# Optimization experiments

Hardware: AMD Instinct MI355X
Metric: run time of the kernel (lower is better)

## Reference

```python
import jax, jax.numpy as jnp
import numpy as np

NH, HS, K = 32, 2048, 16
HD = HS // NH
B, L = 4, 2048
EPS = 1e-6

def _ln(x, gamma, beta):
    mu = x.mean(-1, keepdims=True)
    var = x.var(-1, keepdims=True)  # ddof=0 == torch unbiased=False
    return gamma * ((x - mu) / jnp.sqrt(var + EPS)) + beta

def _ln_fused_l2_bwd(x, target, gamma, beta):
    D = x.shape[-1]
    mu = x.mean(-1, keepdims=True)
    std = jnp.sqrt(x.var(-1, keepdims=True) + EPS)
    xh = (x - mu) / std
    gxh = (gamma * xh + beta - target) * gamma
    return (D * gxh - gxh.sum(-1, keepdims=True) - xh * (gxh * xh).sum(-1, keepdims=True)) / (D * std)

def setup_inputs() -> dict:
    key = jax.random.key(0)
    ks = jax.random.split(key, 8)
    s = 0.02
    return {
        'hidden_states': jax.random.normal(ks[0], (B, L, HS), jnp.float32),
        'position_ids': jnp.tile(jnp.arange(L, dtype=jnp.int32)[None], (B, 1)),
        'q_w': jax.random.normal(ks[1], (HS, HS), jnp.float32) * s,
        'k_w': jax.random.normal(ks[2], (HS, HS), jnp.float32) * s,
        'v_w': jax.random.normal(ks[3], (HS, HS), jnp.float32) * s,
        'o_w': jax.random.normal(ks[4], (HS, HS), jnp.float32) * s,
        'W1': jax.random.normal(ks[5], (NH, HD, HD), jnp.float32) * s,
        'b1': jnp.zeros((NH, 1, HD), jnp.float32),
        'ttt_norm_weight': jnp.ones((NH, HD), jnp.float32),
        'ttt_norm_bias': jnp.zeros((NH, HD), jnp.float32),
        'ttt_lr_weight': jax.random.normal(ks[6], (NH, 1, HS), jnp.float32) * s,
        'ttt_lr_bias': jnp.zeros((NH, 1), jnp.float32),
        'learnable_token_idx': jnp.zeros((K,), jnp.float32),
        'post_norm_weight': jnp.ones((HS,), jnp.float32),
        'post_norm_bias': jnp.zeros((HS,), jnp.float32),
    }

def _forward(hidden_states, q_w, k_w, v_w, o_w, W1, b1, ttt_norm_weight,
             ttt_norm_bias, ttt_lr_weight, ttt_lr_bias, learnable_token_idx,
             post_norm_weight, post_norm_bias):
    Bb, Ll, _ = hidden_states.shape
    NM = Ll // K

    def proj_heads(w):
        return (hidden_states @ w.T).reshape(Bb, Ll, NH, HD).transpose(0, 2, 1, 3)

    XQ = proj_heads(q_w).reshape(Bb, NH, NM, K, HD)
    XK = proj_heads(k_w).reshape(Bb, NH, NM, K, HD)
    XV = proj_heads(v_w).reshape(Bb, NH, NM, K, HD)
    X = hidden_states.reshape(Bb, NM, K, HS)

    # eta: learned per-token lr gate, [B,nh,NM,K,K]
    ttt_lr = jnp.einsum('bnkc,hdc->bhnkd', X, ttt_lr_weight) + ttt_lr_bias.reshape(1, NH, 1, 1, 1)
    ttt_lr_eta = jax.nn.sigmoid(ttt_lr).transpose(0, 1, 2, 4, 3) / HD  # ttt_base_lr = 1.0
    token_idx = jnp.clip(1.0 / jnp.arange(1, K + 1, dtype=jnp.float32) + learnable_token_idx, 0.0, None)
    eta = token_idx.reshape(1, 1, 1, K, 1) * ttt_lr_eta

    ln_w = ttt_norm_weight.reshape(NH, 1, HD)
    ln_b = ttt_norm_bias.reshape(NH, 1, HD)

    def step(carry, x):
        W1_s, b1_s = carry                 # [B,nh,hd,hd], [B,nh,1,hd]
        xq, xk, xv, eta_mb = x             # [B,nh,K,hd], eta_mb [B,nh,K,K]
        Z1 = xk @ W1_s + b1_s
        grad = _ln_fused_l2_bwd(Z1, xv - xk, ln_w, ln_b)
        Attn1 = jnp.tril(xq @ xk.swapaxes(-1, -2))
        b1_bar = b1_s - jnp.tril(eta_mb) @ grad
        Z1_bar = xq @ W1_s - (eta_mb * Attn1) @ grad + b1_bar
        last_eta = eta_mb[:, :, -1, :, None]  # [B,nh,K,1]
        W1_new = W1_s - (last_eta * xk).swapaxes(-1, -2) @ grad
        b1_new = b1_s - jnp.sum(last_eta * grad, axis=-2, keepdims=True)
        out = xq + _ln(Z1_bar, ln_w, ln_b)
        return (W1_new, b1_new), out

    init = (jnp.tile(W1[None], (Bb, 1, 1, 1)), jnp.tile(b1[None], (Bb, 1, 1, 1)))
    xs = (XQ.transpose(2, 0, 1, 3, 4), XK.transpose(2, 0, 1, 3, 4),
          XV.transpose(2, 0, 1, 3, 4), eta.transpose(2, 0, 1, 3, 4))
    _, ys = jax.lax.scan(step, init, xs)          # [NM,B,nh,K,hd]
    out = ys.transpose(1, 0, 3, 2, 4).reshape(Bb, Ll, HS)
    out = _ln(out, post_norm_weight, post_norm_bias)  # post_norm (eps 1e-6)
    return out @ o_w.T

def reference(hidden_states, position_ids, q_w, k_w, v_w, o_w, W1, b1,
              ttt_norm_weight, ttt_norm_bias, ttt_lr_weight, ttt_lr_bias,
              learnable_token_idx, post_norm_weight, post_norm_bias):
    del position_ids  # unused in the shown forward (rope never applied)
    return _forward(hidden_states, q_w, k_w, v_w, o_w, W1, b1, ttt_norm_weight,
                    ttt_norm_bias, ttt_lr_weight, ttt_lr_bias, learnable_token_idx,
                    post_norm_weight, post_norm_bias)
```

## Files before the change

kernel.cpp:

```cpp
#include <hip/hip_runtime.h>

typedef unsigned short u16;
typedef unsigned int u32;
typedef __bf16 bf16_t;
typedef bf16_t bf16x4 __attribute__((ext_vector_type(4)));
typedef bf16_t bf16x8 __attribute__((ext_vector_type(8)));
typedef float f32x4 __attribute__((ext_vector_type(4)));
typedef u16 u16x4 __attribute__((ext_vector_type(4)));
typedef u16 u16x8 __attribute__((ext_vector_type(8)));
typedef short s16x4 __attribute__((ext_vector_type(4)));

#define B_   4
#define L_   2048
#define HS_  2048
#define NH_  32
#define HD_  64
#define KK_  16
#define NM_  128
#define M_   (B_*L_)

__device__ __forceinline__ u16 f2bf(float f) {
  unsigned u = __float_as_uint(f);
  u += 0x7FFFu + ((u >> 16) & 1u);
  return (u16)(u >> 16);
}
__device__ __forceinline__ float bf2f(u16 u) {
  return __uint_as_float(((unsigned)u) << 16);
}
__device__ __forceinline__ u16 f2bfh(float f) {
  __bf16 h = (__bf16)f;
  return __builtin_bit_cast(u16, h);
}
__device__ __forceinline__ s16x4 pk4(float a, float b, float c, float d) {
  bf16x4 v;
  v[0] = (__bf16)a; v[1] = (__bf16)b; v[2] = (__bf16)c; v[3] = (__bf16)d;
  return __builtin_bit_cast(s16x4, v);
}

__device__ __forceinline__ f32x4 mfma16(s16x4 a, s16x4 b, f32x4 c) {
  return __builtin_amdgcn_mfma_f32_16x16x16bf16_1k(a, b, c, 0, 0, 0);
}

template <int CTRL>
__device__ __forceinline__ float dpp_add(float v) {
  int t = __builtin_amdgcn_update_dpp(0, __builtin_bit_cast(int, v), CTRL, 0xF, 0xF, true);
  return v + __builtin_bit_cast(float, t);
}
template <int CTRL>
__device__ __forceinline__ f32x4 dpp_add4(f32x4 v) {
  f32x4 r;
#pragma unroll
  for (int i = 0; i < 4; ++i) r[i] = dpp_add<CTRL>(v[i]);
  return r;
}
__device__ __forceinline__ f32x4 row_reduce16(f32x4 v) {
  v = dpp_add4<0x121>(v);
  v = dpp_add4<0x122>(v);
  v = dpp_add4<0x124>(v);
  v = dpp_add4<0x128>(v);
  return v;
}

__global__ __launch_bounds__(256) void cast_f32_bf16(const float* __restrict__ in,
                                                     u16* __restrict__ out, int n) {
  int i = (blockIdx.x * 256 + threadIdx.x) * 8;
  if (i >= n) return;
  float4 a = *(const float4*)(in + i);
  float4 b = *(const float4*)(in + i + 4);
  u16x8 o;
  o[0]=f2bf(a.x); o[1]=f2bf(a.y); o[2]=f2bf(a.z); o[3]=f2bf(a.w);
  o[4]=f2bf(b.x); o[5]=f2bf(b.y); o[6]=f2bf(b.z); o[7]=f2bf(b.w);
  *(u16x8*)(out + i) = o;
}

#define BM 128
#define BN 128
#define BK 32
#define LDT 40

template <bool BF16OUT>
__global__ __launch_bounds__(256) void gemm_nt(const u16* __restrict__ A,
                                               const u16* __restrict__ Bt,
                                               void* __restrict__ Cv,
                                               int M, int N, int K) {
  __shared__ u16 As[BM * LDT];
  __shared__ u16 Bs[BN * LDT];
  int tid  = threadIdx.x;
  int lane = tid & 63, wave = tid >> 6;
  int quad = lane >> 4, l16 = lane & 15;
  int bM = blockIdx.x * BM, bN = blockIdx.y * BN;
  int wM = (wave >> 1) * 64, wN = (wave & 1) * 64;
  int r0 = tid >> 2, c0 = (tid & 3) * 8;
  const u16* Ap = A + (size_t)bM * K;
  const u16* Bp = Bt + (size_t)bN * K;
  f32x4 acc[4][4] = {};
  u16x8 pa0 = *(const u16x8*)(Ap + (size_t)r0 * K + c0);
  u16x8 pa1 = *(const u16x8*)(Ap + (size_t)(r0 + 64) * K + c0);
  u16x8 pb0 = *(const u16x8*)(Bp + (size_t)r0 * K + c0);
  u16x8 pb1 = *(const u16x8*)(Bp + (size_t)(r0 + 64) * K + c0);
  int nk = K / BK;
  for (int kt = 0; kt < nk; ++kt) {
    *(u16x8*)&As[r0 * LDT + c0]        = pa0;
    *(u16x8*)&As[(r0 + 64) * LDT + c0] = pa1;
    *(u16x8*)&Bs[r0 * LDT + c0]        = pb0;
    *(u16x8*)&Bs[(r0 + 64) * LDT + c0] = pb1;
    __syncthreads();
    if (kt + 1 < nk) {
      int k0 = (kt + 1) * BK + c0;
      pa0 = *(const u16x8*)(Ap + (size_t)r0 * K + k0);
      pa1 = *(const u16x8*)(Ap + (size_t)(r0 + 64) * K + k0);
      pb0 = *(const u16x8*)(Bp + (size_t)r0 * K + k0);
      pb1 = *(const u16x8*)(Bp + (size_t)(r0 + 64) * K + k0);
    }
    bf16x8 af[4], bfr[4];
#pragma unroll
    for (int i = 0; i < 4; ++i) {
      u16x8 t = *(const u16x8*)&As[(wM + i * 16 + l16) * LDT + quad * 8];
      af[i] = __builtin_bit_cast(bf16x8, t);
    }
#pragma unroll
    for (int j = 0; j < 4; ++j) {
      u16x8 t = *(const u16x8*)&Bs[(wN + j * 16 + l16) * LDT + quad * 8];
      bfr[j] = __builtin_bit_cast(bf16x8, t);
    }
#pragma unroll
    for (int i = 0; i < 4; ++i) {
#pragma unroll
      for (int j = 0; j < 4; ++j)
        acc[i][j] = __builtin_amdgcn_mfma_f32_16x16x32_bf16(af[i], bfr[j], acc[i][j], 0, 0, 0);
    }
    __syncthreads();
  }
#pragma unroll
  for (int i = 0; i < 4; ++i) {
#pragma unroll
    for (int j = 0; j < 4; ++j) {
      int row = bM + wM + i * 16 + quad * 4;
      int col = bN + wN + j * 16 + l16;
      if (BF16OUT) {
        u16* cp = (u16*)Cv + (size_t)row * N + col;
#pragma unroll
        for (int r = 0; r < 4; ++r) cp[(size_t)r * N] = f2bf(acc[i][j][r]);
      } else {
        float* cp = (float*)Cv + (size_t)row * N + col;
#pragma unroll
        for (int r = 0; r < 4; ++r) cp[(size_t)r * N] = acc[i][j][r];
      }
    }
  }
}

__global__ __launch_bounds__(256) void sig_kernel(const u16* __restrict__ hsb,
                                                  const u16* __restrict__ lrwb,
                                                  const float* __restrict__ lrb,
                                                  float* __restrict__ Sig) {
  __shared__ u16 Bs[32 * LDT];
  int tid = threadIdx.x;
  int lane = tid & 63, wave = tid >> 6;
  int quad = lane >> 4, l16 = lane & 15;
  int m0 = blockIdx.x * 64 + wave * 16;
  f32x4 acc0 = {}, acc1 = {};
  for (int kt = 0; kt < HS_ / BK; ++kt) {
    int k0 = kt * BK;
    if (tid < 128) {
      int r = tid >> 2, c8 = (tid & 3) * 8;
      *(u16x8*)&Bs[r * LDT + c8] = *(const u16x8*)(lrwb + (size_t)r * HS_ + k0 + c8);
    }
    __syncthreads();
    u16x8 ta = *(const u16x8*)(hsb + (size_t)(m0 + l16) * HS_ + k0 + quad * 8);
    u16x8 t0 = *(const u16x8*)&Bs[l16 * LDT + quad * 8];
    u16x8 t1 = *(const u16x8*)&Bs[(16 + l16) * LDT + quad * 8];
    bf16x8 af  = __builtin_bit_cast(bf16x8, ta);
    bf16x8 bf0 = __builtin_bit_cast(bf16x8, t0);
    bf16x8 bf1 = __builtin_bit_cast(bf16x8, t1);
    acc0 = __builtin_amdgcn_mfma_f32_16x16x32_bf16(af, bf0, acc0, 0, 0, 0);
    acc1 = __builtin_amdgcn_mfma_f32_16x16x32_bf16(af, bf1, acc1, 0, 0, 0);
    __syncthreads();
  }
#pragma unroll
  for (int j = 0; j < 2; ++j) {
    f32x4 a = j ? acc1 : acc0;
    int h = j * 16 + l16;
    float bias = lrb[h];
#pragma unroll
    for (int r = 0; r < 4; ++r) {
      int m = m0 + quad * 4 + r;
      float v = a[r] + bias;
      float s = (1.f / (1.f + expf(-v))) * (1.f / 64.f);
      Sig[(size_t)m * NH_ + h] = s;
    }
  }
}

__global__ __launch_bounds__(64, 1) void ttt_scan_wave(
    const u16* __restrict__ XQ, const u16* __restrict__ XK, const u16* __restrict__ XV,
    const float* __restrict__ Sig, const float* __restrict__ W1_0, const float* __restrict__ b1_0,
    const float* __restrict__ lnw, const float* __restrict__ lnb, const float* __restrict__ lti,
    float* __restrict__ Y) {
  __shared__ __align__(16) u16 xkT[64 * 20];
  __shared__ __align__(16) float diffS[16 * 68];

  int lane = threadIdx.x;
  int quad = lane >> 4, l16 = lane & 15;
  int bh = blockIdx.x, b = bh >> 5, h = bh & 31;

  f32x4 m2[4][4];
  {
    const float* wsrc = W1_0 + (size_t)h * 4096;
#pragma unroll
    for (int c = 0; c < 4; ++c)
#pragma unroll
      for (int a = 0; a < 4; ++a)
#pragma unroll
        for (int r = 0; r < 4; ++r)
          m2[c][a][r] = wsrc[(size_t)(c * 16 + quad * 4 + r) * 64 + a * 16 + l16];
  }

  f32x4 b1r, gam, bet;
#pragma unroll
  for (int a = 0; a < 4; ++a) {
    b1r[a] = b1_0[h * 64 + a * 16 + l16];
    gam[a] = lnw[h * 64 + a * 16 + l16];
    bet[a] = lnb[h * 64 + a * 16 + l16];
  }
  float tokL  = fmaxf(1.0f / (float)(l16 + 1) + lti[l16], 0.0f);
  float tok15 = fmaxf(1.0f / 16.0f + lti[15], 0.0f);

  size_t gb = ((size_t)(b * L_ + l16)) * HS_ + h * HD_ + quad * 4;
  const float* sigp = Sig + (size_t)(b * L_ + quad * 4) * NH_ + h;

  u16x4 cxk[4], cxq[4], cxv[4];
  f32x4 csig;
#pragma unroll
  for (int c = 0; c < 4; ++c) {
    cxk[c] = *(const u16x4*)(XK + gb + c * 16);
    cxq[c] = *(const u16x4*)(XQ + gb + c * 16);
    cxv[c] = *(const u16x4*)(XV + gb + c * 16);
  }
#pragma unroll
  for (int r = 0; r < 4; ++r) csig[r] = sigp[(size_t)r * NH_];

  for (int n = 0; n < NM_; ++n) {
    s16x4 fwB[4][4];
#pragma unroll
    for (int c = 0; c < 4; ++c)
#pragma unroll
      for (int a = 0; a < 4; ++a)
        fwB[c][a] = pk4(m2[c][a][0], m2[c][a][1], m2[c][a][2], m2[c][a][3]);

#pragma unroll
    for (int c = 0; c < 4; ++c) {
      f32x4 dv;
#pragma unroll
      for (int j = 0; j < 4; ++j) dv[j] = bf2f(cxv[c][j]) - bf2f(cxk[c][j]);
      *(f32x4*)&diffS[l16 * 68 + c * 16 + quad * 4] = dv;
#pragma unroll
      for (int j = 0; j < 4; ++j)
        xkT[(c * 16 + quad * 4 + j) * 20 + l16] = f2bfh(-tok15 * bf2f(cxk[c][j]));
    }

    s16x4 fxk[4], fxq[4];
#pragma unroll
    for (int c = 0; c < 4; ++c) {
      fxk[c] = __builtin_bit_cast(s16x4, cxk[c]);
      fxq[c] = __builtin_bit_cast(s16x4, cxq[c]);
    }
    f32x4 sigc = csig;

    if (n + 1 < NM_) {
      size_t g = gb + (size_t)(n + 1) * KK_ * HS_;
#pragma unroll
      for (int c = 0; c < 4; ++c) {
        cxk[c] = *(const u16x4*)(XK + g + c * 16);
        cxq[c] = *(const u16x4*)(XQ + g + c * 16);
        cxv[c] = *(const u16x4*)(XV + g + c * 16);
      }
#pragma unroll
      for (int r = 0; r < 4; ++r)
        csig[r] = sigp[(size_t)((n + 1) * KK_ + r) * NH_];
    }

    f32x4 z1[4] = {}, zq4[4] = {}, atT = {};
#pragma unroll
    for (int c = 0; c < 4; ++c) {
      atT = mfma16(fxk[c], fxq[c], atT);
#pragma unroll
      for (int a = 0; a < 4; ++a) {
        z1[a]  = mfma16(fxk[c], fwB[c][a], z1[a]);
        zq4[a] = mfma16(fxq[c], fwB[c][a], zq4[a]);
      }
    }

    float cf[4];
#pragma unroll
    for (int r = 0; r < 4; ++r)
      cf[r] = (quad * 4 + r <= l16) ? -tokL * (1.0f + atT[r]) : 0.0f;
    s16x4 fA = pk4(cf[0], cf[1], cf[2], cf[3]);

#pragma unroll
    for (int a = 0; a < 4; ++a)
#pragma unroll
      for (int r = 0; r < 4; ++r) z1[a][r] += b1r[a];
    f32x4 s1 = z1[0] + z1[1] + z1[2] + z1[3];
    f32x4 s2 = z1[0] * z1[0] + z1[1] * z1[1] + z1[2] * z1[2] + z1[3] * z1[3];
    s1 = row_reduce16(s1);
    s2 = row_reduce16(s2);
    f32x4 mu, rstd;
#pragma unroll
    for (int r = 0; r < 4; ++r) {
      mu[r] = s1[r] * (1.0f / 64.0f);
      float var = s2[r] * (1.0f / 64.0f) - mu[r] * mu[r];
      rstd[r] = 1.0f / sqrtf(var + 1e-6f);
    }

    f32x4 dd[4];
#pragma unroll
    for (int a = 0; a < 4; ++a)
#pragma unroll
      for (int r = 0; r < 4; ++r)
        dd[a][r] = diffS[(quad * 4 + r) * 68 + a * 16 + l16];

    f32x4 xh[4], gxh[4], t1v = {}, t2v = {};
#pragma unroll
    for (int a = 0; a < 4; ++a) {
#pragma unroll
      for (int r = 0; r < 4; ++r) {
        xh[a][r]  = (z1[a][r] - mu[r]) * rstd[r];
        gxh[a][r] = (gam[a] * xh[a][r] + bet[a] - dd[a][r]) * gam[a];
      }
      t1v = t1v + gxh[a];
      t2v = t2v + gxh[a] * xh[a];
    }
    t1v = row_reduce16(t1v);
    t2v = row_reduce16(t2v);

    s16x4 fG[4];
    float bs[4];
#pragma unroll
    for (int a = 0; a < 4; ++a) {
      float sg[4];
#pragma unroll
      for (int r = 0; r < 4; ++r) {
        float g = (64.0f * gxh[a][r] - t1v[r] - xh[a][r] * t2v[r]) * (rstd[r] * (1.0f / 64.0f));
        sg[r] = sigc[r] * g;
      }
      fG[a] = pk4(sg[0], sg[1], sg[2], sg[3]);
      bs[a] = sg[0] + sg[1] + sg[2] + sg[3];
    }
#pragma unroll
    for (int a = 0; a < 4; ++a) {
      bs[a] += __shfl_xor(bs[a], 16, 64);
      bs[a] += __shfl_xor(bs[a], 32, 64);
    }

    f32x4 zb[4];
#pragma unroll
    for (int a = 0; a < 4; ++a) {
      zb[a] = mfma16(fA, fG[a], zq4[a]);
#pragma unroll
      for (int r = 0; r < 4; ++r) zb[a][r] += b1r[a];
    }
#pragma unroll
    for (int a = 0; a < 4; ++a) b1r[a] -= tok15 * bs[a];

    {
      s16x4 fX[4];
#pragma unroll
      for (int c = 0; c < 4; ++c)
        fX[c] = *(const s16x4*)&xkT[(c * 16 + l16) * 20 + quad * 4];
#pragma unroll
      for (int c = 0; c < 4; ++c)
#pragma unroll
        for (int a = 0; a < 4; ++a)
          m2[c][a] = mfma16(fX[c], fG[a], m2[c][a]);
    }

    f32x4 w1s = zb[0] + zb[1] + zb[2] + zb[3];
    f32x4 w2s = zb[0] * zb[0] + zb[1] * zb[1] + zb[2] * zb[2] + zb[3] * zb[3];
    w1s = row_reduce16(w1s);
    w2s = row_reduce16(w2s);
#pragma unroll
    for (int r = 0; r < 4; ++r) {
      float mu2 = w1s[r] * (1.0f / 64.0f);
      float var2 = w2s[r] * (1.0f / 64.0f) - mu2 * mu2;
      float rstd2 = 1.0f / sqrtf(var2 + 1e-6f);
      float* yp = Y + ((size_t)(b * L_ + n * KK_ + quad * 4 + r)) * HS_ + h * HD_ + l16;
#pragma unroll
      for (int a = 0; a < 4; ++a)
        yp[a * 16] = gam[a] * ((zb[a][r] - mu2) * rstd2) + bet[a];
    }
  }
}

__global__ __launch_bounds__(256) void postnorm(const float* __restrict__ Yin,
                                                const u16* __restrict__ XQr,
                                                const float* __restrict__ w,
                                                const float* __restrict__ bb,
                                                u16* __restrict__ Yn) {
  __shared__ float red[8];
  int row = blockIdx.x, tid = threadIdx.x;
  const float* x = Yin + (size_t)row * HS_ + tid * 8;
  float4 v0 = *(const float4*)(x);
  float4 v1 = *(const float4*)(x + 4);
  u16x8 xqv = *(const u16x8*)(XQr + (size_t)row * HS_ + tid * 8);
  float vals[8] = {v0.x, v0.y, v0.z, v0.w, v1.x, v1.y, v1.z, v1.w};
#pragma unroll
  for (int t = 0; t < 8; ++t) vals[t] += bf2f(xqv[t]);
  float s = 0.f, ss = 0.f;
#pragma unroll
  for (int t = 0; t < 8; ++t) { s += vals[t]; ss += vals[t] * vals[t]; }
#pragma unroll
  for (int m = 32; m > 0; m >>= 1) { s += __shfl_xor(s, m, 64); ss += __shfl_xor(ss, m, 64); }
  int wave = tid >> 6, lane = tid & 63;
  if (lane == 0) { red[wave] = s; red[4 + wave] = ss; }
  __syncthreads();
  float S  = red[0] + red[1] + red[2] + red[3];
  float SS = red[4] + red[5] + red[6] + red[7];
  float mu = S * (1.f / 2048.f);
  float var = SS * (1.f / 2048.f) - mu * mu;
  float rstd = 1.f / sqrtf(var + 1e-6f);
  const float* wp = w + tid * 8;
  const float* bp = bb + tid * 8;
  u16x8 o;
#pragma unroll
  for (int t = 0; t < 8; ++t) o[t] = f2bf(wp[t] * ((vals[t] - mu) * rstd) + bp[t]);
  *(u16x8*)(Yn + (size_t)row * HS_ + tid * 8) = o;
}

extern "C" void kernel_launch(void* const* d_in, const int* in_sizes, int n_in,
                              void* d_out, int out_size, void* d_ws, size_t ws_size,
                              hipStream_t stream) {
  (void)in_sizes; (void)n_in; (void)out_size; (void)ws_size;
  const float* hidden = (const float*)d_in[0];
  const float* q_w = (const float*)d_in[2];
  const float* k_w = (const float*)d_in[3];
  const float* v_w = (const float*)d_in[4];
  const float* o_w = (const float*)d_in[5];
  const float* W1  = (const float*)d_in[6];
  const float* b1i = (const float*)d_in[7];
  const float* lnw = (const float*)d_in[8];
  const float* lnb = (const float*)d_in[9];
  const float* lrw = (const float*)d_in[10];
  const float* lrb = (const float*)d_in[11];
  const float* lti = (const float*)d_in[12];
  const float* pnw = (const float*)d_in[13];
  const float* pnb = (const float*)d_in[14];
  float* out = (float*)d_out;

  char* w = (char*)d_ws;
  u16* hsb  = (u16*)w;  w += (size_t)16777216 * 2;
  u16* wb   = (u16*)w;  w += (size_t)4194304 * 2;
  u16* lrwb = (u16*)w;  w += (size_t)65536 * 2;
  u16* XQb  = (u16*)w;  w += (size_t)16777216 * 2;
  u16* XKb  = (u16*)w;  w += (size_t)16777216 * 2;
  u16* XVb  = (u16*)w;  w += (size_t)16777216 * 2;
  float* Sg = (float*)w; w += (size_t)M_ * NH_ * 4;
  u16* Yn = hsb;

  cast_f32_bf16<<<8192, 256, 0, stream>>>(hidden, hsb, 16777216);
  cast_f32_bf16<<<32, 256, 0, stream>>>(lrw, lrwb, 65536);

  sig_kernel<<<128, 256, 0, stream>>>(hsb, lrwb, lrb, Sg);

  dim3 gg(M_ / BM, HS_ / BN);
  cast_f32_bf16<<<2048, 256, 0, stream>>>(q_w, wb, 4194304);
  gemm_nt<true><<<gg, 256, 0, stream>>>(hsb, wb, XQb, M_, HS_, HS_);
  cast_f32_bf16<<<2048, 256, 0, stream>>>(k_w, wb, 4194304);
  gemm_nt<true><<<gg, 256, 0, stream>>>(hsb, wb, XKb, M_, HS_, HS_);
  cast_f32_bf16<<<2048, 256, 0, stream>>>(v_w, wb, 4194304);
  gemm_nt<true><<<gg, 256, 0, stream>>>(hsb, wb, XVb, M_, HS_, HS_);

  ttt_scan_wave<<<128, 64, 0, stream>>>(XQb, XKb, XVb, Sg, W1, b1i, lnw, lnb, lti, out);

  postnorm<<<8192, 256, 0, stream>>>(out, XQb, pnw, pnb, Yn);

  cast_f32_bf16<<<2048, 256, 0, stream>>>(o_w, wb, 4194304);
  gemm_nt<false><<<gg, 256, 0, stream>>>(Yn, wb, out, M_, HS_, HS_);
}
```

Measured before the change: 893.0 us.

## Interleave two independent head scans per wave to hide serial latency

Each wave now carries two (batch, head) recurrent chains and interleaves their per-chunk work, with the grid halved from 128 to 64 single-wave blocks. The aim is to fill the dependency stalls of the serial scan (MFMA chains, row reductions, shuffles, LDS round trips) with independent work from the second chain. The cost is roughly double the register footprint, since the W1 state alone takes 128 VGPRs per chain, which risks spills. It also halves the number of CUs in use, so each wave must gain enough ILP to offset running on half as many units.

Result: slower. 1.253 ms (+40.3%).

```diff
diff --git a/kernel.cpp b/kernel.cpp
--- a/kernel.cpp
+++ b/kernel.cpp
@@ -197,15 +197,23 @@
     const float* __restrict__ Sig, const float* __restrict__ W1_0, const float* __restrict__ b1_0,
     const float* __restrict__ lnw, const float* __restrict__ lnb, const float* __restrict__ lti,
     float* __restrict__ Y) {
-  __shared__ __align__(16) u16 xkT[64 * 20];
-  __shared__ __align__(16) float diffS[16 * 68];
+  __shared__ __align__(16) u16 xkT[2][64 * 20];
+  __shared__ __align__(16) float diffS[2][16 * 68];
 
   int lane = threadIdx.x;
   int quad = lane >> 4, l16 = lane & 15;
-  int bh = blockIdx.x, b = bh >> 5, h = bh & 31;
-
-  f32x4 m2[4][4];
-  {
+
+  f32x4 m2[2][4][4];
+  f32x4 b1r[2], gam[2], bet[2];
+  size_t gb[2];
+  const float* sigp[2];
+  float* yb[2];
+  u16x4 cxk[2][4], cxq[2][4], cxv[2][4];
+  f32x4 csig[2];
+
+#pragma unroll
+  for (int ch = 0; ch < 2; ++ch) {
+    int bh = blockIdx.x * 2 + ch, b = bh >> 5, h = bh & 31;
     const float* wsrc = W1_0 + (size_t)h * 4096;
 #pragma unroll
     for (int c = 0; c < 4; ++c)
@@ -213,181 +221,203 @@
       for (int a = 0; a < 4; ++a)
 #pragma unroll
         for (int r = 0; r < 4; ++r)
-          m2[c][a][r] = wsrc[(size_t)(c * 16 + quad * 4 + r) * 64 + a * 16 + l16];
+          m2[ch][c][a][r] = wsrc[(size_t)(c * 16 + quad * 4 + r) * 64 + a * 16 + l16];
+#pragma unroll
+    for (int a = 0; a < 4; ++a) {
+      b1r[ch][a] = b1_0[h * 64 + a * 16 + l16];
+      gam[ch][a] = lnw[h * 64 + a * 16 + l16];
+      bet[ch][a] = lnb[h * 64 + a * 16 + l16];
+    }
+    gb[ch]   = ((size_t)(b * L_ + l16)) * HS_ + h * HD_ + quad * 4;
+    sigp[ch] = Sig + (size_t)(b * L_ + quad * 4) * NH_ + h;
+    yb[ch]   = Y + (size_t)(b * L_) * HS_ + h * HD_ + l16;
+#pragma unroll
+    for (int c = 0; c < 4; ++c) {
+      cxk[ch][c] = *(const u16x4*)(XK + gb[ch] + c * 16);
+      cxq[ch][c] = *(const u16x4*)(XQ + gb[ch] + c * 16);
+      cxv[ch][c] = *(const u16x4*)(XV + gb[ch] + c * 16);
+    }
+#pragma unroll
+    for (int r = 0; r < 4; ++r) csig[ch][r] = sigp[ch][(size_t)r * NH_];
   }
 
-  f32x4 b1r, gam, bet;
-#pragma unroll
-  for (int a = 0; a < 4; ++a) {
-    b1r[a] = b1_0[h * 64 + a * 16 + l16];
-    gam[a] = lnw[h * 64 + a * 16 + l16];
-    bet[a] = lnb[h * 64 + a * 16 + l16];
-  }
   float tokL  = fmaxf(1.0f / (float)(l16 + 1) + lti[l16], 0.0f);
   float tok15 = fmaxf(1.0f / 16.0f + lti[15], 0.0f);
 
-  size_t gb = ((size_t)(b * L_ + l16)) * HS_ + h * HD_ + quad * 4;
-  const float* sigp = Sig + (size_t)(b * L_ + quad * 4) * NH_ + h;
-
-  u16x4 cxk[4], cxq[4], cxv[4];
-  f32x4 csig;
-#pragma unroll
-  for (int c = 0; c < 4; ++c) {
-    cxk[c] = *(const u16x4*)(XK + gb + c * 16);
-    cxq[c] = *(const u16x4*)(XQ + gb + c * 16);
-    cxv[c] = *(const u16x4*)(XV + gb + c * 16);
-  }
-#pragma unroll
-  for (int r = 0; r < 4; ++r) csig[r] = sigp[(size_t)r * NH_];
-
   for (int n = 0; n < NM_; ++n) {
-    s16x4 fwB[4][4];
-#pragma unroll
-    for (int c = 0; c < 4; ++c)
+    s16x4 fwB[2][4][4];
+#pragma unroll
+    for (int ch = 0; ch < 2; ++ch)
+#pragma unroll
+      for (int c = 0; c < 4; ++c)
+#pragma unroll
+        for (int a = 0; a < 4; ++a)
+          fwB[ch][c][a] = pk4(m2[ch][c][a][0], m2[ch][c][a][1], m2[ch][c][a][2], m2[ch][c][a][3]);
+
+#pragma unroll
+    for (int ch = 0; ch < 2; ++ch)
+#pragma unroll
+      for (int c = 0; c < 4; ++c) {
+        f32x4 dv;
+#pragma unroll
+        for (int j = 0; j < 4; ++j) dv[j] = bf2f(cxv[ch][c][j]) - bf2f(cxk[ch][c][j]);
+        *(f32x4*)&diffS[ch][l16 * 68 + c * 16 + quad * 4] = dv;
+#pragma unroll
+        for (int j = 0; j < 4; ++j)
+          xkT[ch][(c * 16 + quad * 4 + j) * 20 + l16] = f2bfh(-tok15 * bf2f(cxk[ch][c][j]));
+      }
+
+    f32x4 sigc[2] = {csig[0], csig[1]};
+
+    f32x4 z1[2][4] = {}, zq4[2][4] = {}, atT[2] = {};
+#pragma unroll
+    for (int ch = 0; ch < 2; ++ch)
+#pragma unroll
+      for (int c = 0; c < 4; ++c) {
+        s16x4 fxk = __builtin_bit_cast(s16x4, cxk[ch][c]);
+        s16x4 fxq = __builtin_bit_cast(s16x4, cxq[ch][c]);
+        atT[ch] = mfma16(fxk, fxq, atT[ch]);
+#pragma unroll
+        for (int a = 0; a < 4; ++a) {
+          z1[ch][a]  = mfma16(fxk, fwB[ch][c][a], z1[ch][a]);
+          zq4[ch][a] = mfma16(fxq, fwB[ch][c][a], zq4[ch][a]);
+        }
+      }
+
+    if (n + 1 < NM_) {
+#pragma unroll
+      for (int ch = 0; ch < 2; ++ch) {
+        size_t g = gb[ch] + (size_t)(n + 1) * KK_ * HS_;
+#pragma unroll
+        for (int c = 0; c < 4; ++c) {
+          cxk[ch][c] = *(const u16x4*)(XK + g + c * 16);
+          cxq[ch][c] = *(const u16x4*)(XQ + g + c * 16);
+          cxv[ch][c] = *(const u16x4*)(XV + g + c * 16);
+        }
+#pragma unroll
+        for (int r = 0; r < 4; ++r)
+          csig[ch][r] = sigp[ch][(size_t)((n + 1) * KK_ + r) * NH_];
+      }
+    }
+
+    s16x4 fA[2];
+#pragma unroll
+    for (int ch = 0; ch < 2; ++ch) {
+      float cf[4];
+#pragma unroll
+      for (int r = 0; r < 4; ++r)
+        cf[r] = (quad * 4 + r <= l16) ? -tokL * (1.0f + atT[ch][r]) : 0.0f;
+      fA[ch] = pk4(cf[0], cf[1], cf[2], cf[3]);
+    }
+
+    f32x4 mu[2], rstd[2];
+#pragma unroll
+    for (int ch = 0; ch < 2; ++ch) {
 #pragma unroll
       for (int a = 0; a < 4; ++a)
-        fwB[c][a] = pk4(m2[c][a][0], m2[c][a][1], m2[c][a][2], m2[c][a][3]);
-
-#pragma unroll
-    for (int c = 0; c < 4; ++c) {
-      f32x4 dv;
-#pragma unroll
-      for (int j = 0; j < 4; ++j) dv[j] = bf2f(cxv[c][j]) - bf2f(cxk[c][j]);
-      *(f32x4*)&diffS[l16 * 68 + c * 16 + quad * 4] = dv;
-#pragma unroll
-      for (int j = 0; j < 4; ++j)
-        xkT[(c * 16 + quad * 4 + j) * 20 + l16] = f2bfh(-tok15 * bf2f(cxk[c][j]));
-    }
-
-    s16x4 fxk[4], fxq[4];
-#pragma unroll
-    for (int c = 0; c < 4; ++c) {
-      fxk[c] = __builtin_bit_cast(s16x4, cxk[c]);
-      fxq[c] = __builtin_bit_cast(s16x4, cxq[c]);
-    }
-    f32x4 sigc = csig;
-
-    if (n + 1 < NM_) {
-      size_t g = gb + (size_t)(n + 1) * KK_ * HS_;
-#pragma unroll
-      for (int c = 0; c < 4; ++c) {
-        cxk[c] = *(const u16x4*)(XK + g + c * 16);
-        cxq[c] = *(const u16x4*)(XQ + g + c * 16);
-        cxv[c] = *(const u16x4*)(XV + g + c * 16);
-      }
-#pragma unroll
-      for (int r = 0; r < 4; ++r)
-        csig[r] = sigp[(size_t)((n + 1) * KK_ + r) * NH_];
-    }
-
-    f32x4 z1[4] = {}, zq4[4] = {}, atT = {};
-#pragma unroll
-    for (int c = 0; c < 4; ++c) {
-      atT = mfma16(fxk[c], fxq[c], atT);
+#pragma unroll
+        for (int r = 0; r < 4; ++r) z1[ch][a][r] += b1r[ch][a];
+      f32x4 s1 = z1[ch][0] + z1[ch][1] + z1[ch][2] + z1[ch][3];
+      f32x4 s2 = z1[ch][0] * z1[ch][0] + z1[ch][1] * z1[ch][1]
+               + z1[ch][2] * z1[ch][2] + z1[ch][3] * z1[ch][3];
+      s1 = row_reduce16(s1);
+      s2 = row_reduce16(s2);
+#pragma unroll
+      for (int r = 0; r < 4; ++r) {
+        mu[ch][r] = s1[r] * (1.0f / 64.0f);
+        float var = s2[r] * (1.0f / 64.0f) - mu[ch][r] * mu[ch][r];
+        rstd[ch][r] = 1.0f / sqrtf(var + 1e-6f);
+      }
+    }
+
+    f32x4 xh[2][4], gxh[2][4], t1v[2], t2v[2];
+#pragma unroll
+    for (int ch = 0; ch < 2; ++ch) {
+      f32x4 a1 = {}, a2 = {};
 #pragma unroll
       for (int a = 0; a < 4; ++a) {
-        z1[a]  = mfma16(fxk[c], fwB[c][a], z1[a]);
-        zq4[a] = mfma16(fxq[c], fwB[c][a], zq4[a]);
-      }
-    }
-
-    float cf[4];
-#pragma unroll
-    for (int r = 0; r < 4; ++r)
-      cf[r] = (quad * 4 + r <= l16) ? -tokL * (1.0f + atT[r]) : 0.0f;
-    s16x4 fA = pk4(cf[0], cf[1], cf[2], cf[3]);
-
-#pragma unroll
-    for (int a = 0; a < 4; ++a)
-#pragma unroll
-      for (int r = 0; r < 4; ++r) z1[a][r] += b1r[a];
-    f32x4 s1 = z1[0] + z1[1] + z1[2] + z1[3];
-    f32x4 s2 = z1[0] * z1[0] + z1[1] * z1[1] + z1[2] * z1[2] + z1[3] * z1[3];
-    s1 = row_reduce16(s1);
-    s2 = row_reduce16(s2);
-    f32x4 mu, rstd;
-#pragma unroll
-    for (int r = 0; r < 4; ++r) {
-      mu[r] = s1[r] * (1.0f / 64.0f);
-      float var = s2[r] * (1.0f / 64.0f) - mu[r] * mu[r];
-      rstd[r] = 1.0f / sqrtf(var + 1e-6f);
-    }
-
-    f32x4 dd[4];
-#pragma unroll
-    for (int a = 0; a < 4; ++a)
-#pragma unroll
-      for (int r = 0; r < 4; ++r)
-        dd[a][r] = diffS[(quad * 4 + r) * 68 + a * 16 + l16];
-
-    f32x4 xh[4], gxh[4], t1v = {}, t2v = {};
-#pragma unroll
-    for (int a = 0; a < 4; ++a) {
+        f32x4 dd;
+#pragma unroll
+        for (int r = 0; r < 4; ++r)
+          dd[r] = diffS[ch][(quad * 4 + r) * 68 + a * 16 + l16];
+#pragma unroll
+        for (int r = 0; r < 4; ++r) {
+          xh[ch][a][r]  = (z1[ch][a][r] - mu[ch][r]) * rstd[ch][r];
+          gxh[ch][a][r] = (gam[ch][a] * xh[ch][a][r] + bet[ch][a] - dd[r]) * gam[ch][a];
+        }
+        a1 = a1 + gxh[ch][a];
+        a2 = a2 + gxh[ch][a] * xh[ch][a];
+      }
+      t1v[ch] = row_reduce16(a1);
+      t2v[ch] = row_reduce16(a2);
+    }
+
+    s16x4 fG[2][4];
+    f32x4 bsv[2];
+#pragma unroll
+    for (int ch = 0; ch < 2; ++ch) {
+#pragma unroll
+      for (int a = 0; a < 4; ++a) {
+        float sg[4];
+#pragma unroll
+        for (int r = 0; r < 4; ++r) {
+          float g = (64.0f * gxh[ch][a][r] - t1v[ch][r] - xh[ch][a][r] * t2v[ch][r])
+                    * (rstd[ch][r] * (1.0f / 64.0f));
+          sg[r] = sigc[ch][r] * g;
+        }
+        fG[ch][a] = pk4(sg[0], sg[1], sg[2], sg[3]);
+        bsv[ch][a] = sg[0] + sg[1] + sg[2] + sg[3];
+      }
+#pragma unroll
+      for (int a = 0; a < 4; ++a) {
+        bsv[ch][a] += __shfl_xor(bsv[ch][a], 16, 64);
+        bsv[ch][a] += __shfl_xor(bsv[ch][a], 32, 64);
+      }
+    }
+
+    f32x4 zb[2][4];
+#pragma unroll
+    for (int ch = 0; ch < 2; ++ch) {
+#pragma unroll
+      for (int a = 0; a < 4; ++a) {
+        zb[ch][a] = mfma16(fA[ch], fG[ch][a], zq4[ch][a]);
+#pragma unroll
+        for (int r = 0; r < 4; ++r) zb[ch][a][r] += b1r[ch][a];
+      }
+#pragma unroll
+      for (int a = 0; a < 4; ++a) b1r[ch][a] -= tok15 * bsv[ch][a];
+    }
+
+#pragma unroll
+    for (int ch = 0; ch < 2; ++ch) {
+      s16x4 fX[4];
+#pragma unroll
+      for (int c = 0; c < 4; ++c)
+        fX[c] = *(const s16x4*)&xkT[ch][(c * 16 + l16) * 20 + quad * 4];
+#pragma unroll
+      for (int c = 0; c < 4; ++c)
+#pragma unroll
+        for (int a = 0; a < 4; ++a)
+          m2[ch][c][a] = mfma16(fX[c], fG[ch][a], m2[ch][c][a]);
+    }
+
+#pragma unroll
+    for (int ch = 0; ch < 2; ++ch) {
+      f32x4 w1s = zb[ch][0] + zb[ch][1] + zb[ch][2] + zb[ch][3];
+      f32x4 w2s = zb[ch][0] * zb[ch][0] + zb[ch][1] * zb[ch][1]
+                + zb[ch][2] * zb[ch][2] + zb[ch][3] * zb[ch][3];
+      w1s = row_reduce16(w1s);
+      w2s = row_reduce16(w2s);
 #pragma unroll
       for (int r = 0; r < 4; ++r) {
-        xh[a][r]  = (z1[a][r] - mu[r]) * rstd[r];
-        gxh[a][r] = (gam[a] * xh[a][r] + bet[a] - dd[a][r]) * gam[a];
-      }
-      t1v = t1v + gxh[a];
-      t2v = t2v + gxh[a] * xh[a];
-    }
-    t1v = row_reduce16(t1v);
-    t2v = row_reduce16(t2v);
-
-    s16x4 fG[4];
-    float bs[4];
-#pragma unroll
-    for (int a = 0; a < 4; ++a) {
-      float sg[4];
-#pragma unroll
-      for (int r = 0; r < 4; ++r) {
-        float g = (64.0f * gxh[a][r] - t1v[r] - xh[a][r] * t2v[r]) * (rstd[r] * (1.0f / 64.0f));
-        sg[r] = sigc[r] * g;
-      }
-      fG[a] = pk4(sg[0], sg[1], sg[2], sg[3]);
-      bs[a] = sg[0] + sg[1] + sg[2] + sg[3];
-    }
-#pragma unroll
-    for (int a = 0; a < 4; ++a) {
-      bs[a] += __shfl_xor(bs[a], 16, 64);
-      bs[a] += __shfl_xor(bs[a], 32, 64);
-    }
-
-    f32x4 zb[4];
-#pragma unroll
-    for (int a = 0; a < 4; ++a) {
-      zb[a] = mfma16(fA, fG[a], zq4[a]);
-#pragma unroll
-      for (int r = 0; r < 4; ++r) zb[a][r] += b1r[a];
-    }
-#pragma unroll
-    for (int a = 0; a < 4; ++a) b1r[a] -= tok15 * bs[a];
-
-    {
-      s16x4 fX[4];
-#pragma unroll
-      for (int c = 0; c < 4; ++c)
-        fX[c] = *(const s16x4*)&xkT[(c * 16 + l16) * 20 + quad * 4];
-#pragma unroll
-      for (int c = 0; c < 4; ++c)
+        float mu2 = w1s[r] * (1.0f / 64.0f);
+        float var2 = w2s[r] * (1.0f / 64.0f) - mu2 * mu2;
+        float rstd2 = 1.0f / sqrtf(var2 + 1e-6f);
+        float* yp = yb[ch] + (size_t)(n * KK_ + quad * 4 + r) * HS_;
 #pragma unroll
         for (int a = 0; a < 4; ++a)
-          m2[c][a] = mfma16(fX[c], fG[a], m2[c][a]);
-    }
-
-    f32x4 w1s = zb[0] + zb[1] + zb[2] + zb[3];
-    f32x4 w2s = zb[0] * zb[0] + zb[1] * zb[1] + zb[2] * zb[2] + zb[3] * zb[3];
-    w1s = row_reduce16(w1s);
-    w2s = row_reduce16(w2s);
-#pragma unroll
-    for (int r = 0; r < 4; ++r) {
-      float mu2 = w1s[r] * (1.0f / 64.0f);
-      float var2 = w2s[r] * (1.0f / 64.0f) - mu2 * mu2;
-      float rstd2 = 1.0f / sqrtf(var2 + 1e-6f);
-      float* yp = Y + ((size_t)(b * L_ + n * KK_ + quad * 4 + r)) * HS_ + h * HD_ + l16;
-#pragma unroll
-      for (int a = 0; a < 4; ++a)
-        yp[a * 16] = gam[a] * ((zb[a][r] - mu2) * rstd2) + bet[a];
+          yp[a * 16] = gam[ch][a] * ((zb[ch][a][r] - mu2) * rstd2) + bet[ch][a];
+      }
     }
   }
 }
@@ -470,7 +500,7 @@
   cast_f32_bf16<<<2048, 256, 0, stream>>>(v_w, wb, 4194304);
   gemm_nt<true><<<gg, 256, 0, stream>>>(hsb, wb, XVb, M_, HS_, HS_);
 
-  ttt_scan_wave<<<128, 64, 0, stream>>>(XQb, XKb, XVb, Sg, W1, b1i, lnw, lnb, lti, out);
+  ttt_scan_wave<<<64, 64, 0, stream>>>(XQb, XKb, XVb, Sg, W1, b1i, lnw, lnb, lti, out);
 
   postnorm<<<8192, 256, 0, stream>>>(out, XQb, pnw, pnb, Yn);
 
```

## Load GEMM tiles straight to LDS with double buffering and fragment-major layout

Applied to the files above, without the earlier changes.

The NT GEMM now uses global_load_lds to move A and B tiles from global memory straight into shared memory, skipping the register staging step. Shared memory is double-buffered, so the next K-tile loads while MFMAs run on the current one, and one of the two barriers per iteration is dropped. Tiles are stored fragment-major, 512 contiguous elements per 16x32 block, so each lane reads its 16 bytes without padding or bank conflicts. Shared memory doubles, and correctness relies on the barrier also waiting for the asynchronous LDS loads.

After: 1.119 ms. +25.3%, slower.

```diff
diff --git a/kernel.cpp b/kernel.cpp
--- a/kernel.cpp
+++ b/kernel.cpp
@@ -39,6 +39,11 @@
 
 __device__ __forceinline__ f32x4 mfma16(s16x4 a, s16x4 b, f32x4 c) {
   return __builtin_amdgcn_mfma_f32_16x16x16bf16_1k(a, b, c, 0, 0, 0);
+}
+
+__device__ __forceinline__ void gload_lds16(const u16* g, u16* l) {
+  __builtin_amdgcn_global_load_lds((const __attribute__((address_space(1))) void*)g,
+                                   (__attribute__((address_space(3))) void*)l, 16, 0, 0);
 }
 
 template <int CTRL>
@@ -76,51 +81,52 @@
 #define BM 128
 #define BN 128
 #define BK 32
-#define LDT 40
 
 template <bool BF16OUT>
 __global__ __launch_bounds__(256) void gemm_nt(const u16* __restrict__ A,
                                                const u16* __restrict__ Bt,
                                                void* __restrict__ Cv,
                                                int M, int N, int K) {
-  __shared__ u16 As[BM * LDT];
-  __shared__ u16 Bs[BN * LDT];
+  __shared__ u16 As[2][BM * BK];
+  __shared__ u16 Bs[2][BN * BK];
   int tid  = threadIdx.x;
   int lane = tid & 63, wave = tid >> 6;
   int quad = lane >> 4, l16 = lane & 15;
   int bM = blockIdx.x * BM, bN = blockIdx.y * BN;
   int wM = (wave >> 1) * 64, wN = (wave & 1) * 64;
-  int r0 = tid >> 2, c0 = (tid & 3) * 8;
-  const u16* Ap = A + (size_t)bM * K;
-  const u16* Bp = Bt + (size_t)bN * K;
+  int wMb = (wave >> 1) * 4, wNb = (wave & 1) * 4;
+
+  int bi0 = wave * 2;
+  const u16* gA0 = A  + (size_t)(bM + bi0 * 16 + l16) * K + quad * 8;
+  const u16* gB0 = Bt + (size_t)(bN + bi0 * 16 + l16) * K + quad * 8;
+
   f32x4 acc[4][4] = {};
-  u16x8 pa0 = *(const u16x8*)(Ap + (size_t)r0 * K + c0);
-  u16x8 pa1 = *(const u16x8*)(Ap + (size_t)(r0 + 64) * K + c0);
-  u16x8 pb0 = *(const u16x8*)(Bp + (size_t)r0 * K + c0);
-  u16x8 pb1 = *(const u16x8*)(Bp + (size_t)(r0 + 64) * K + c0);
   int nk = K / BK;
+
+  gload_lds16(gA0,               &As[0][bi0 * 512]);
+  gload_lds16(gA0 + (size_t)16 * K, &As[0][bi0 * 512 + 512]);
+  gload_lds16(gB0,               &Bs[0][bi0 * 512]);
+  gload_lds16(gB0 + (size_t)16 * K, &Bs[0][bi0 * 512 + 512]);
+
+  int cur = 0;
   for (int kt = 0; kt < nk; ++kt) {
-    *(u16x8*)&As[r0 * LDT + c0]        = pa0;
-    *(u16x8*)&As[(r0 + 64) * LDT + c0] = pa1;
-    *(u16x8*)&Bs[r0 * LDT + c0]        = pb0;
-    *(u16x8*)&Bs[(r0 + 64) * LDT + c0] = pb1;
     __syncthreads();
     if (kt + 1 < nk) {
-      int k0 = (kt + 1) * BK + c0;
-      pa0 = *(const u16x8*)(Ap + (size_t)r0 * K + k0);
-      pa1 = *(const u16x8*)(Ap + (size_t)(r0 + 64) * K + k0);
-      pb0 = *(const u16x8*)(Bp + (size_t)r0 * K + k0);
-      pb1 = *(const u16x8*)(Bp + (size_t)(r0 + 64) * K + k0);
+      int k0 = (kt + 1) * BK;
+      gload_lds16(gA0 + k0,                &As[cur ^ 1][bi0 * 512]);
+      gload_lds16(gA0 + (size_t)16 * K + k0, &As[cur ^ 1][bi0 * 512 + 512]);
+      gload_lds16(gB0 + k0,                &Bs[cur ^ 1][bi0 * 512]);
+      gload_lds16(gB0 + (size_t)16 * K + k0, &Bs[cur ^ 1][bi0 * 512 + 512]);
     }
     bf16x8 af[4], bfr[4];
 #pragma unroll
     for (int i = 0; i < 4; ++i) {
-      u16x8 t = *(const u16x8*)&As[(wM + i * 16 + l16) * LDT + quad * 8];
+      u16x8 t = *(const u16x8*)&As[cur][(wMb + i) * 512 + lane * 8];
       af[i] = __builtin_bit_cast(bf16x8, t);
     }
 #pragma unroll
     for (int j = 0; j < 4; ++j) {
-      u16x8 t = *(const u16x8*)&Bs[(wN + j * 16 + l16) * LDT + quad * 8];
+      u16x8 t = *(const u16x8*)&Bs[cur][(wNb + j) * 512 + lane * 8];
       bfr[j] = __builtin_bit_cast(bf16x8, t);
     }
 #pragma unroll
@@ -129,7 +135,7 @@
       for (int j = 0; j < 4; ++j)
         acc[i][j] = __builtin_amdgcn_mfma_f32_16x16x32_bf16(af[i], bfr[j], acc[i][j], 0, 0, 0);
     }
-    __syncthreads();
+    cur ^= 1;
   }
 #pragma unroll
   for (int i = 0; i < 4; ++i) {
@@ -150,6 +156,7 @@
   }
 }
 
+#define LDT 40
 __global__ __launch_bounds__(256) void sig_kernel(const u16* __restrict__ hsb,
                                                   const u16* __restrict__ lrwb,
                                                   const float* __restrict__ lrb,
@@ -160,8 +167,8 @@
   int quad = lane >> 4, l16 = lane & 15;
   int m0 = blockIdx.x * 64 + wave * 16;
   f32x4 acc0 = {}, acc1 = {};
-  for (int kt = 0; kt < HS_ / BK; ++kt) {
-    int k0 = kt * BK;
+  for (int kt = 0; kt < HS_ / 32; ++kt) {
+    int k0 = kt * 32;
     if (tid < 128) {
       int r = tid >> 2, c8 = (tid & 3) * 8;
       *(u16x8*)&Bs[r * LDT + c8] = *(const u16x8*)(lrwb + (size_t)r * HS_ + k0 + c8);
```
